# Performance work log

Measured on AMD Instinct MI355X. Metric: run time of the kernel, lower is better.

## Reference

```python
import jax, jax.numpy as jnp
import numpy as np

B, N, T, C, H, E = 4, 256, 36, 64, 4, 4096
D = C // H          # per-head dim
CH = 2 * C          # GAT hidden channels (embed_size * 2)


def _ln(x, g, b):
    mu = x.mean(-1, keepdims=True)
    v = ((x - mu) ** 2).mean(-1, keepdims=True)
    return (x - mu) / jnp.sqrt(v + 1e-5) * g + b


def _gat_conv(x, src, dst, W, a_s, a_d, b):
    # GATConv, heads=1, add_self_loops=False, negative_slope=0.2
    h = x @ W                                        # [N, F]
    e = jax.nn.leaky_relu((h * a_s).sum(-1)[src] + (h * a_d).sum(-1)[dst], 0.2)  # [E]
    m = jax.ops.segment_max(e, dst, num_segments=N)  # per-dst softmax (stable)
    w = jnp.exp(e - m[dst])
    s = jax.ops.segment_sum(w, dst, num_segments=N)
    alpha = w / (s[dst] + 1e-16)
    return jax.ops.segment_sum(h[src] * alpha[:, None], dst, num_segments=N) + b


def _forward(query, key, value, edge_attr, D_S, W_emb, b_emb, Wq, Wk, Wv, W_fc, b_fc,
             ln1_g, ln1_b, ln2_g, ln2_b, W_ff1, b_ff1, W_ff2, b_ff2,
             gat1_W, gat1_as, gat1_ad, gat1_b, gat2_W, gat2_as, gat2_ad, gat2_b,
             jk_W, jk_b, W_fs, b_fs, W_fg, b_fg, edge_index):
    src, dst = edge_index[0], edge_index[1]

    def gat(x):  # [N, C] -> [N, C]; 2-layer GAT with jk='max'
        h1 = jax.nn.relu(_gat_conv(x, src, dst, gat1_W, gat1_as, gat1_ad, gat1_b))
        h2 = jax.nn.relu(_gat_conv(h1, src, dst, gat2_W, gat2_as, gat2_ad, gat2_b))
        return jnp.maximum(h1, h2) @ jk_W + jk_b

    # GAT is applied to the ORIGINAL query (before D_S is added), once per timestep.
    xg = jax.vmap(jax.vmap(gat))(query.transpose(0, 2, 1, 3))  # [B, T, N, C]
    # source loop PREPENDS each timestep's output -> time axis is reversed
    X_G = xg[:, ::-1].transpose(0, 2, 1, 3)                    # [B, N, T, C]

    ds = (D_S @ W_emb + b_emb)[None, :, None, :]               # [1, N, 1, C]
    q = query + ds
    k = key + ds
    v = value + ds

    qh = q.reshape(B, N, T, H, D) @ Wq                         # per-head shared linear
    kh = k.reshape(B, N, T, H, D) @ Wk
    vh = v.reshape(B, N, T, H, D) @ Wv
    attn = jnp.einsum('bqthd,bkthd->bqkth', qh, kh)            # [B, N, N, T, H]
    # NOTE: source softmaxes over dim=1 (the QUERY axis), scaled by sqrt(embed_size)
    a = jax.nn.softmax(attn / jnp.sqrt(jnp.float32(C)), axis=1)
    o = jnp.einsum('bqkth,bkthd->bqthd', a, vh).reshape(B, N, T, C)
    o = o @ W_fc + b_fc

    M_s = _ln(o + q, ln1_g, ln1_b)                             # dropout p=0 (identity)
    ff = jax.nn.relu(M_s @ W_ff1 + b_ff1) @ W_ff2 + b_ff2
    U_s = _ln(ff + M_s, ln2_g, ln2_b)

    g = jax.nn.sigmoid(U_s @ W_fs + b_fs + X_G @ W_fg + b_fg)
    return g * U_s + (1.0 - g) * X_G


def setup_inputs():
    key = jax.random.key(0)
    ki = iter(jax.random.split(key, 64))

    def p(shape):
        fan = shape[0]
        return jax.random.normal(next(ki), shape, dtype=jnp.float32) / jnp.float32(float(np.sqrt(fan)))

    inp = {}
    inp['query'] = jax.random.normal(next(ki), (B, N, T, C), dtype=jnp.float32)
    inp['key'] = jax.random.normal(next(ki), (B, N, T, C), dtype=jnp.float32)
    inp['value'] = jax.random.normal(next(ki), (B, N, T, C), dtype=jnp.float32)
    inp['edge_attr'] = jax.random.normal(next(ki), (E,), dtype=jnp.float32)
    inp['D_S'] = jax.random.normal(next(ki), (N, N), dtype=jnp.float32)  # adj, learned param
    inp['W_emb'] = p((N, C)); inp['b_emb'] = jnp.zeros((C,), jnp.float32)
    inp['Wq'] = p((D, D)); inp['Wk'] = p((D, D)); inp['Wv'] = p((D, D))
    inp['W_fc'] = p((C, C)); inp['b_fc'] = jnp.zeros((C,), jnp.float32)
    inp['ln1_g'] = jnp.ones((C,), jnp.float32); inp['ln1_b'] = jnp.zeros((C,), jnp.float32)
    inp['ln2_g'] = jnp.ones((C,), jnp.float32); inp['ln2_b'] = jnp.zeros((C,), jnp.float32)
    inp['W_ff1'] = p((C, 4 * C)); inp['b_ff1'] = jnp.zeros((4 * C,), jnp.float32)
    inp['W_ff2'] = p((4 * C, C)); inp['b_ff2'] = jnp.zeros((C,), jnp.float32)
    inp['gat1_W'] = p((C, CH)); inp['gat1_as'] = p((CH,)); inp['gat1_ad'] = p((CH,)); inp['gat1_b'] = jnp.zeros((CH,), jnp.float32)
    inp['gat2_W'] = p((CH, CH)); inp['gat2_as'] = p((CH,)); inp['gat2_ad'] = p((CH,)); inp['gat2_b'] = jnp.zeros((CH,), jnp.float32)
    inp['jk_W'] = p((CH, C)); inp['jk_b'] = jnp.zeros((C,), jnp.float32)
    inp['W_fs'] = p((C, C)); inp['b_fs'] = jnp.zeros((C,), jnp.float32)
    inp['W_fg'] = p((C, C)); inp['b_fg'] = jnp.zeros((C,), jnp.float32)
    inp['edge_index'] = jax.random.randint(next(ki), (2, E), 0, N, dtype=jnp.int32)
    return inp


def reference(query, key, value, edge_attr, D_S, W_emb, b_emb, Wq, Wk, Wv, W_fc, b_fc,
              ln1_g, ln1_b, ln2_g, ln2_b, W_ff1, b_ff1, W_ff2, b_ff2,
              gat1_W, gat1_as, gat1_ad, gat1_b, gat2_W, gat2_as, gat2_ad, gat2_b,
              jk_W, jk_b, W_fs, b_fs, W_fg, b_fg, edge_index):
    return _forward(query, key, value, edge_attr, D_S, W_emb, b_emb, Wq, Wk, Wv, W_fc, b_fc,
                    ln1_g, ln1_b, ln2_g, ln2_b, W_ff1, b_ff1, W_ff2, b_ff2,
                    gat1_W, gat1_as, gat1_ad, gat1_b, gat2_W, gat2_as, gat2_ad, gat2_b,
                    jk_W, jk_b, W_fs, b_fs, W_fg, b_fg, edge_index)
```

## Files before the change

kernel.cpp:

```cpp
#include <hip/hip_runtime.h>

typedef unsigned short u16;
typedef unsigned int u32;

#define B_ 4
#define N_ 256
#define T_ 36
#define C_ 64
#define H_ 4
#define D_ 16
#define CH_ 128
#define E_ 4096
#define G_ (B_*T_)
#define TOK_ (B_*N_*T_)

#define DS_OFF  0
#define XG_OFF  (DS_OFF + N_*C_)
#define HA_OFF  (XG_OFF + TOK_*C_)
#define HB_OFF  (HA_OFF + G_*N_*CH_/2)
#define HS_OFF  (HB_OFF + G_*N_*CH_/2)
#define HD_OFF  (HS_OFF + G_*N_)
#define INT_OFF (HD_OFF + G_*N_)
#define MS_OFF  (INT_OFF + 4608)

__device__ __forceinline__ float bf2f(u16 u){
  u32 x = ((u32)u) << 16;
  return __builtin_bit_cast(float, x);
}
__device__ __forceinline__ u16 f2bf(float f){
  u32 x = __builtin_bit_cast(u32, f);
  x += 0x7fffu + ((x >> 16) & 1u);
  return (u16)(x >> 16);
}
__device__ __forceinline__ void unpack8(uint4 u, float* f){
  f[0]=bf2f((u16)(u.x & 0xffffu)); f[1]=bf2f((u16)(u.x >> 16));
  f[2]=bf2f((u16)(u.y & 0xffffu)); f[3]=bf2f((u16)(u.y >> 16));
  f[4]=bf2f((u16)(u.z & 0xffffu)); f[5]=bf2f((u16)(u.z >> 16));
  f[6]=bf2f((u16)(u.w & 0xffffu)); f[7]=bf2f((u16)(u.w >> 16));
}
__device__ __forceinline__ uint4 pack8f(const float* f){
  uint4 u;
  u.x = (u32)f2bf(f[0]) | ((u32)f2bf(f[1]) << 16);
  u.y = (u32)f2bf(f[2]) | ((u32)f2bf(f[3]) << 16);
  u.z = (u32)f2bf(f[4]) | ((u32)f2bf(f[5]) << 16);
  u.w = (u32)f2bf(f[6]) | ((u32)f2bf(f[7]) << 16);
  return u;
}
__device__ __forceinline__ int rfl(int v){ return __builtin_amdgcn_readfirstlane(v); }

__device__ __forceinline__ void gq_from_bid(int bid, int& g, int& q){
  int xc = bid & 7, slot = bid >> 3;
  q = slot & 3;
  g = xc + ((slot >> 2) << 3);
}

#define SP_ 20

__global__ __launch_bounds__(256)
void k_pre(const float* __restrict__ query, const float* __restrict__ W1,
           const float* __restrict__ as1, const float* __restrict__ ad1,
           u16* __restrict__ h, float* __restrict__ hs_ws, float* __restrict__ hd_ws,
           const float* __restrict__ DSm, const float* __restrict__ Wemb,
           const float* __restrict__ bemb, float* __restrict__ dsb,
           const int* __restrict__ ei, int* __restrict__ indptr, int* __restrict__ srcs)
{
  __shared__ union UP {
    struct { float xs[64][65]; float red[2][4][64]; } lin;
    struct { int srcL[E_]; int dstL[E_]; int tmp[E_]; int cnt[N_]; int base[N_+1]; } c;
  } S;
  const int bid = blockIdx.x;
  const int tid = threadIdx.x;

  if (bid < 576){
    int g, q; gq_from_bid(bid, g, q);
    const int n0 = q * 64;
    const int b = g / T_, t = g % T_;
    {
      const size_t gb = (((size_t)b*N_ + n0)*T_ + t)*C_;
      #pragma unroll
      for (int it = 0; it < 4; it++){
        int idx = tid + 256*it;
        int row = idx >> 4, c4 = (idx & 15) * 4;
        float4 v = *(const float4*)(query + gb + (size_t)row*(T_*C_) + c4);
        S.lin.xs[row][c4+0] = v.x; S.lin.xs[row][c4+1] = v.y;
        S.lin.xs[row][c4+2] = v.z; S.lin.xs[row][c4+3] = v.w;
      }
    }
    __syncthreads();

    const int r = tid & 63;
    const int cb = rfl(tid >> 6);
    const int ch0 = cb * 32;

    float acc[32];
    #pragma unroll
    for (int j = 0; j < 32; j++) acc[j] = 0.f;
    for (int k = 0; k < 64; k++){
      float xv = S.lin.xs[r][k];
      const float* wrow = W1 + k*CH_ + ch0;
      #pragma unroll
      for (int j = 0; j < 32; j++) acc[j] += xv * wrow[j];
    }
    float hs = 0.f, hd = 0.f;
    #pragma unroll
    for (int j = 0; j < 32; j++){ hs += acc[j]*as1[ch0+j]; hd += acc[j]*ad1[ch0+j]; }
    S.lin.red[0][cb][r] = hs; S.lin.red[1][cb][r] = hd;

    u16* hp = h + ((size_t)(g*N_ + n0 + r))*CH_ + ch0;
    #pragma unroll
    for (int j8 = 0; j8 < 32; j8 += 8)
      *(uint4*)(hp + j8) = pack8f(&acc[j8]);

    __syncthreads();
    if (tid < 64){
      float a = S.lin.red[0][0][tid]+S.lin.red[0][1][tid]+S.lin.red[0][2][tid]+S.lin.red[0][3][tid];
      float d = S.lin.red[1][0][tid]+S.lin.red[1][1][tid]+S.lin.red[1][2][tid]+S.lin.red[1][3][tid];
      hs_ws[g*N_ + n0 + tid] = a;
      hd_ws[g*N_ + n0 + tid] = d;
    }
  } else if (bid < 640){
    const int n = (bid - 576) * 4 + (tid >> 6);
    const int c = tid & 63;
    float acc = bemb[c];
    for (int m = 0; m < N_; m++) acc += DSm[n*N_ + m] * Wemb[m*C_ + c];
    dsb[n*C_ + c] = acc;
  } else {
    for (int e = tid; e < E_; e += 256){ S.c.srcL[e] = ei[e]; S.c.dstL[e] = ei[E_ + e]; }
    S.c.cnt[tid] = 0;
    __syncthreads();
    for (int e = tid; e < E_; e += 256) atomicAdd(&S.c.cnt[S.c.dstL[e]], 1);
    __syncthreads();
    if (tid == 0){
      int run = 0;
      for (int i = 0; i < N_; i++){ S.c.base[i] = run; run += S.c.cnt[i]; }
      S.c.base[N_] = run;
    }
    __syncthreads();
    S.c.cnt[tid] = 0;
    __syncthreads();
    for (int e = tid; e < E_; e += 256){
      int d = S.c.dstL[e];
      int p = atomicAdd(&S.c.cnt[d], 1);
      S.c.tmp[S.c.base[d] + p] = e;
    }
    __syncthreads();
    {
      const int p0 = S.c.base[tid], p1 = S.c.base[tid] + S.c.cnt[tid];
      for (int i = p0 + 1; i < p1; i++){
        int v = S.c.tmp[i]; int j = i - 1;
        while (j >= p0 && S.c.tmp[j] > v){ S.c.tmp[j+1] = S.c.tmp[j]; j--; }
        S.c.tmp[j+1] = v;
      }
      for (int j = p0; j < p1; j++) srcs[j] = S.c.srcL[S.c.tmp[j]];
    }
    indptr[tid] = S.c.base[tid];
    if (tid == 0) indptr[N_] = S.c.base[N_];
  }
}

__global__ __launch_bounds__(256)
void k_agg1(const u16* __restrict__ hin, const float* __restrict__ hs_ws, const float* __restrict__ hd_ws,
            const int* __restrict__ indptr, const int* __restrict__ srcs,
            const float* __restrict__ bias, u16* __restrict__ hout)
{
  __shared__ int   srcs_l[E_];
  __shared__ float alpha_l[E_];
  __shared__ float hs_l[N_];
  const int bid = blockIdx.x;
  int g, q; gq_from_bid(bid, g, q);
  const int n0 = q * 64;
  const int tid = threadIdx.x;

  const int p00 = indptr[n0];
  const int pend = indptr[n0 + 64];
  const int cntE = pend - p00;
  for (int i = tid; i < cntE; i += 256) srcs_l[i] = srcs[p00 + i];
  hs_l[tid] = hs_ws[g*N_ + tid];
  __syncthreads();

  if (tid < 64){
    const int dst = n0 + tid;
    const int p0 = indptr[dst] - p00, p1 = indptr[dst+1] - p00;
    const float hdn = hd_ws[g*N_ + dst];
    for (int j = p0; j < p1; j++){
      float e = hs_l[srcs_l[j]] + hdn;
      alpha_l[j] = e > 0.f ? e : 0.2f * e;
    }
    float m = -1e30f;
    for (int j = p0; j < p1; j++) m = fmaxf(m, alpha_l[j]);
    float s = 0.f;
    for (int j = p0; j < p1; j++){
      float w = __expf(alpha_l[j] - m);
      alpha_l[j] = w; s += w;
    }
    float inv = 1.f / (s + 1e-16f);
    for (int j = p0; j < p1; j++) alpha_l[j] *= inv;
  }
  __syncthreads();

  const int r = tid & 63;
  const int cb = rfl(tid >> 6);
  const int ch0 = cb * 32;
  const int dst = n0 + r;
  const int p0 = indptr[dst] - p00, p1 = indptr[dst+1] - p00;

  float acc[32];
  #pragma unroll
  for (int j = 0; j < 32; j++) acc[j] = 0.f;
  for (int j = p0; j < p1; j++){
    float a = alpha_l[j];
    int s = srcs_l[j];
    const uint4* hp = (const uint4*)(hin + ((size_t)(g*N_ + s))*CH_ + ch0);
    #pragma unroll
    for (int qq = 0; qq < 4; qq++){
      float hv[8]; unpack8(hp[qq], hv);
      #pragma unroll
      for (int i = 0; i < 8; i++) acc[qq*8+i] += a * hv[i];
    }
  }
  float o[32];
  #pragma unroll
  for (int j = 0; j < 32; j++){
    float v = acc[j] + bias[ch0+j];
    o[j] = v > 0.f ? v : 0.f;
  }
  u16* op = hout + ((size_t)(g*N_ + dst))*CH_ + ch0;
  #pragma unroll
  for (int j8 = 0; j8 < 32; j8 += 8)
    *(uint4*)(op + j8) = pack8f(&o[j8]);
}

__global__ __launch_bounds__(256)
void k_lin2(const u16* __restrict__ h1, const float* __restrict__ W2,
            const float* __restrict__ as2, const float* __restrict__ ad2,
            u16* __restrict__ h2, float* __restrict__ hs_ws, float* __restrict__ hd_ws)
{
  __shared__ float xs[64][129];
  __shared__ float red[2][4][64];
  const int bid = blockIdx.x;
  int g, q; gq_from_bid(bid, g, q);
  const int n0 = q * 64;
  const int tid = threadIdx.x;

  {
    #pragma unroll
    for (int it = 0; it < 4; it++){
      int idx = tid + 256*it;
      int row = idx >> 4, c8 = (idx & 15) * 8;
      uint4 u = *(const uint4*)(h1 + ((size_t)(g*N_ + n0 + row))*CH_ + c8);
      float v[8]; unpack8(u, v);
      #pragma unroll
      for (int i = 0; i < 8; i++) xs[row][c8+i] = v[i];
    }
  }
  __syncthreads();

  const int r = tid & 63;
  const int cb = rfl(tid >> 6);
  const int ch0 = cb * 32;

  float acc[32];
  #pragma unroll
  for (int j = 0; j < 32; j++) acc[j] = 0.f;
  for (int k = 0; k < 128; k++){
    float xv = xs[r][k];
    const float* wrow = W2 + k*CH_ + ch0;
    #pragma unroll
    for (int j = 0; j < 32; j++) acc[j] += xv * wrow[j];
  }
  float hs = 0.f, hd = 0.f;
  #pragma unroll
  for (int j = 0; j < 32; j++){ hs += acc[j]*as2[ch0+j]; hd += acc[j]*ad2[ch0+j]; }
  red[0][cb][r] = hs; red[1][cb][r] = hd;

  u16* hp = h2 + ((size_t)(g*N_ + n0 + r))*CH_ + ch0;
  #pragma unroll
  for (int j8 = 0; j8 < 32; j8 += 8)
    *(uint4*)(hp + j8) = pack8f(&acc[j8]);

  __syncthreads();
  if (tid < 64){
    float a = red[0][0][tid]+red[0][1][tid]+red[0][2][tid]+red[0][3][tid];
    float d = red[1][0][tid]+red[1][1][tid]+red[1][2][tid]+red[1][3][tid];
    hs_ws[g*N_ + n0 + tid] = a;
    hd_ws[g*N_ + n0 + tid] = d;
  }
}

__global__ __launch_bounds__(256)
void k_aggjk(const u16* __restrict__ h2, const float* __restrict__ hs_ws, const float* __restrict__ hd_ws,
             const int* __restrict__ indptr, const int* __restrict__ srcs,
             const float* __restrict__ b2, const u16* __restrict__ h1,
             const float* __restrict__ jkW, const float* __restrict__ jkb, float* __restrict__ xg,
             const float* __restrict__ query, const float* __restrict__ key,
             const float* __restrict__ Wq, const float* __restrict__ Wk,
             const float* __restrict__ dsb, float* __restrict__ mS)
{
  __shared__ union UJ {
    struct { int srcs_l[E_]; float alpha_l[E_]; float hs_l[N_]; } a;
    struct { float xs[64][129]; } l;
    struct { float qs[N_][SP_]; float wq[16][16]; float wk[16][16]; } s;
  } U;
  const int bid = blockIdx.x;
  const int tid = threadIdx.x;

  if (bid < 576){
    int g, q; gq_from_bid(bid, g, q);
    const int n0 = q * 64;
    const int b = g / T_, t = g % T_;

    const int p00 = indptr[n0];
    const int pend = indptr[n0 + 64];
    const int cntE = pend - p00;
    for (int i = tid; i < cntE; i += 256) U.a.srcs_l[i] = srcs[p00 + i];
    U.a.hs_l[tid] = hs_ws[g*N_ + tid];
    __syncthreads();

    if (tid < 64){
      const int dst = n0 + tid;
      const int p0 = indptr[dst] - p00, p1 = indptr[dst+1] - p00;
      const float hdn = hd_ws[g*N_ + dst];
      for (int j = p0; j < p1; j++){
        float e = U.a.hs_l[U.a.srcs_l[j]] + hdn;
        U.a.alpha_l[j] = e > 0.f ? e : 0.2f * e;
      }
      float m = -1e30f;
      for (int j = p0; j < p1; j++) m = fmaxf(m, U.a.alpha_l[j]);
      float s = 0.f;
      for (int j = p0; j < p1; j++){
        float w = __expf(U.a.alpha_l[j] - m);
        U.a.alpha_l[j] = w; s += w;
      }
      float inv = 1.f / (s + 1e-16f);
      for (int j = p0; j < p1; j++) U.a.alpha_l[j] *= inv;
    }
    __syncthreads();

    const int r = tid & 63;
    const int cb = rfl(tid >> 6);
    const int ch0 = cb * 32;
    const int dst = n0 + r;
    const int p0 = indptr[dst] - p00, p1 = indptr[dst+1] - p00;

    float acc[32];
    #pragma unroll
    for (int j = 0; j < 32; j++) acc[j] = 0.f;
    for (int j = p0; j < p1; j++){
      float a = U.a.alpha_l[j];
      int s = U.a.srcs_l[j];
      const uint4* hp = (const uint4*)(h2 + ((size_t)(g*N_ + s))*CH_ + ch0);
      #pragma unroll
      for (int qq = 0; qq < 4; qq++){
        float hv[8]; unpack8(hp[qq], hv);
        #pragma unroll
        for (int i = 0; i < 8; i++) acc[qq*8+i] += a * hv[i];
      }
    }
    float o[32];
    {
      const uint4* h1p = (const uint4*)(h1 + ((size_t)(g*N_ + dst))*CH_ + ch0);
      #pragma unroll
      for (int j8 = 0; j8 < 32; j8 += 8){
        float h1v[8]; unpack8(h1p[j8>>3], h1v);
        #pragma unroll
        for (int i = 0; i < 8; i++){
          float v = acc[j8+i] + b2[ch0+j8+i];
          v = v > 0.f ? v : 0.f;
          o[j8+i] = fmaxf(h1v[i], v);
        }
      }
    }
    __syncthreads();

    #pragma unroll
    for (int j = 0; j < 32; j++) U.l.xs[r][ch0+j] = o[j];
    __syncthreads();

    const int o0 = cb * 16;
    float acc2[16];
    #pragma unroll
    for (int j = 0; j < 16; j++) acc2[j] = 0.f;
    for (int k = 0; k < 128; k++){
      float xv = U.l.xs[r][k];
      const float* wrow = jkW + k*C_ + o0;
      #pragma unroll
      for (int j = 0; j < 16; j++) acc2[j] += xv * wrow[j];
    }
    float* op = xg + ((((size_t)b*N_ + n0 + r)*T_) + (T_-1-t))*C_ + o0;
    #pragma unroll
    for (int j4 = 0; j4 < 16; j4 += 4){
      float4 v = make_float4(acc2[j4]+jkb[o0+j4], acc2[j4+1]+jkb[o0+j4+1],
                             acc2[j4+2]+jkb[o0+j4+2], acc2[j4+3]+jkb[o0+j4+3]);
      *(float4*)(op + j4) = v;
    }
  } else {
    const int sb = bid - 576;
    const int b = sb / (T_*H_);
    const int rem = sb % (T_*H_);
    const int t = rem / H_;
    const int h = rem % H_;
    const int n = tid;

    U.s.wq[n>>4][n&15] = Wq[n];
    U.s.wk[n>>4][n&15] = Wk[n];

    const size_t base = ((((size_t)b*N_ + n)*T_) + t)*C_ + h*D_;
    const float* dsp = dsb + n*C_ + h*D_;

    float x[16];
    #pragma unroll
    for (int j4 = 0; j4 < 16; j4 += 4){
      float4 a = *(const float4*)(query + base + j4);
      float4 d = *(const float4*)(dsp + j4);
      x[j4]=a.x+d.x; x[j4+1]=a.y+d.y; x[j4+2]=a.z+d.z; x[j4+3]=a.w+d.w;
    }
    __syncthreads();
    #pragma unroll
    for (int j = 0; j < 16; j++){
      float a = 0.f;
      #pragma unroll
      for (int i = 0; i < 16; i++) a += x[i]*U.s.wq[i][j];
      U.s.qs[n][j] = a;
    }
    float khr[16];
    #pragma unroll
    for (int j4 = 0; j4 < 16; j4 += 4){
      float4 a = *(const float4*)(key + base + j4);
      float4 d = *(const float4*)(dsp + j4);
      x[j4]=a.x+d.x; x[j4+1]=a.y+d.y; x[j4+2]=a.z+d.z; x[j4+3]=a.w+d.w;
    }
    #pragma unroll
    for (int j = 0; j < 16; j++){
      float a = 0.f;
      #pragma unroll
      for (int i = 0; i < 16; i++) a += x[i]*U.s.wk[i][j];
      khr[j] = a;
    }
    __syncthreads();

    float m[4], s[4];
    #pragma unroll
    for (int c = 0; c < 4; c++){ m[c] = -1e30f; s[c] = 0.f; }
    for (int qq = 0; qq < 64; qq++){
      #pragma unroll
      for (int c = 0; c < 4; c++){
        const float* qrow = &U.s.qs[qq + 64*c][0];
        float4 a0 = *(const float4*)(qrow);
        float4 a1 = *(const float4*)(qrow+4);
        float4 a2 = *(const float4*)(qrow+8);
        float4 a3 = *(const float4*)(qrow+12);
        float d = a0.x*khr[0]+a0.y*khr[1]+a0.z*khr[2]+a0.w*khr[3]
                + a1.x*khr[4]+a1.y*khr[5]+a1.z*khr[6]+a1.w*khr[7]
                + a2.x*khr[8]+a2.y*khr[9]+a2.z*khr[10]+a2.w*khr[11]
                + a3.x*khr[12]+a3.y*khr[13]+a3.z*khr[14]+a3.w*khr[15];
        d *= 0.125f;
        float mn = fmaxf(m[c], d);
        s[c] = s[c]*__expf(m[c]-mn) + __expf(d-mn);
        m[c] = mn;
      }
    }
    float M = fmaxf(fmaxf(m[0],m[1]), fmaxf(m[2],m[3]));
    float S = s[0]*__expf(m[0]-M) + s[1]*__expf(m[1]-M)
            + s[2]*__expf(m[2]-M) + s[3]*__expf(m[3]-M);
    mS[(size_t)sb*512 + n*2]     = M;
    mS[(size_t)sb*512 + n*2 + 1] = 1.f / S;
  }
}

__global__ __launch_bounds__(256)
void k_av(const float* __restrict__ query, const float* __restrict__ key, const float* __restrict__ value,
          const float* __restrict__ Wq, const float* __restrict__ Wk, const float* __restrict__ Wv,
          const float* __restrict__ dsb, const float* __restrict__ mS, float* __restrict__ o_ws)
{
  __shared__ float ks[N_][SP_];
  __shared__ float vs[N_][SP_];
  __shared__ float2 msl[N_];
  __shared__ float wq[16][16], wk[16][16], wv[16][16];

  const int bx = blockIdx.x;
  const int b = bx / (T_*H_);
  const int rem = bx % (T_*H_);
  const int t = rem / H_;
  const int h = rem % H_;
  const int n = threadIdx.x;

  wq[n>>4][n&15] = Wq[n];
  wk[n>>4][n&15] = Wk[n];
  wv[n>>4][n&15] = Wv[n];
  msl[n] = *(const float2*)(mS + (size_t)bx*512 + n*2);

  const size_t base = ((((size_t)b*N_ + n)*T_) + t)*C_ + h*D_;
  const float* dsp = dsb + n*C_ + h*D_;

  float ds16[16];
  #pragma unroll
  for (int j4 = 0; j4 < 16; j4 += 4){
    float4 d = *(const float4*)(dsp + j4);
    ds16[j4]=d.x; ds16[j4+1]=d.y; ds16[j4+2]=d.z; ds16[j4+3]=d.w;
  }
  __syncthreads();

  float x[16];
  #pragma unroll
  for (int j4 = 0; j4 < 16; j4 += 4){
    float4 a = *(const float4*)(key + base + j4);
    x[j4]=a.x+ds16[j4]; x[j4+1]=a.y+ds16[j4+1]; x[j4+2]=a.z+ds16[j4+2]; x[j4+3]=a.w+ds16[j4+3];
  }
  #pragma unroll
  for (int j = 0; j < 16; j++){
    float a = 0.f;
    #pragma unroll
    for (int i = 0; i < 16; i++) a += x[i]*wk[i][j];
    ks[n][j] = a;
  }
  #pragma unroll
  for (int j4 = 0; j4 < 16; j4 += 4){
    float4 a = *(const float4*)(value + base + j4);
    x[j4]=a.x+ds16[j4]; x[j4+1]=a.y+ds16[j4+1]; x[j4+2]=a.z+ds16[j4+2]; x[j4+3]=a.w+ds16[j4+3];
  }
  #pragma unroll
  for (int j = 0; j < 16; j++){
    float a = 0.f;
    #pragma unroll
    for (int i = 0; i < 16; i++) a += x[i]*wv[i][j];
    vs[n][j] = a;
  }
  float qhr[16];
  #pragma unroll
  for (int j4 = 0; j4 < 16; j4 += 4){
    float4 a = *(const float4*)(query + base + j4);
    x[j4]=a.x+ds16[j4]; x[j4+1]=a.y+ds16[j4+1]; x[j4+2]=a.z+ds16[j4+2]; x[j4+3]=a.w+ds16[j4+3];
  }
  #pragma unroll
  for (int j = 0; j < 16; j++){
    float a = 0.f;
    #pragma unroll
    for (int i = 0; i < 16; i++) a += x[i]*wq[i][j];
    qhr[j] = a;
  }
  __syncthreads();

  float o0[16], o1[16];
  #pragma unroll
  for (int j = 0; j < 16; j++){ o0[j] = 0.f; o1[j] = 0.f; }
  for (int k = 0; k < N_; k += 2){
    {
      const float* krow = &ks[k][0];
      float4 a0 = *(const float4*)(krow);
      float4 a1 = *(const float4*)(krow+4);
      float4 a2 = *(const float4*)(krow+8);
      float4 a3 = *(const float4*)(krow+12);
      float d = a0.x*qhr[0]+a0.y*qhr[1]+a0.z*qhr[2]+a0.w*qhr[3]
              + a1.x*qhr[4]+a1.y*qhr[5]+a1.z*qhr[6]+a1.w*qhr[7]
              + a2.x*qhr[8]+a2.y*qhr[9]+a2.z*qhr[10]+a2.w*qhr[11]
              + a3.x*qhr[12]+a3.y*qhr[13]+a3.z*qhr[14]+a3.w*qhr[15];
      float2 ms0 = msl[k];
      float p = __expf(d*0.125f - ms0.x) * ms0.y;
      const float* vrow = &vs[k][0];
      float4 v0 = *(const float4*)(vrow);
      float4 v1 = *(const float4*)(vrow+4);
      float4 v2 = *(const float4*)(vrow+8);
      float4 v3 = *(const float4*)(vrow+12);
      o0[0]+=p*v0.x; o0[1]+=p*v0.y; o0[2]+=p*v0.z; o0[3]+=p*v0.w;
      o0[4]+=p*v1.x; o0[5]+=p*v1.y; o0[6]+=p*v1.z; o0[7]+=p*v1.w;
      o0[8]+=p*v2.x; o0[9]+=p*v2.y; o0[10]+=p*v2.z; o0[11]+=p*v2.w;
      o0[12]+=p*v3.x; o0[13]+=p*v3.y; o0[14]+=p*v3.z; o0[15]+=p*v3.w;
    }
    {
      const float* krow = &ks[k+1][0];
      float4 a0 = *(const float4*)(krow);
      float4 a1 = *(const float4*)(krow+4);
      float4 a2 = *(const float4*)(krow+8);
      float4 a3 = *(const float4*)(krow+12);
      float d = a0.x*qhr[0]+a0.y*qhr[1]+a0.z*qhr[2]+a0.w*qhr[3]
              + a1.x*qhr[4]+a1.y*qhr[5]+a1.z*qhr[6]+a1.w*qhr[7]
              + a2.x*qhr[8]+a2.y*qhr[9]+a2.z*qhr[10]+a2.w*qhr[11]
              + a3.x*qhr[12]+a3.y*qhr[13]+a3.z*qhr[14]+a3.w*qhr[15];
      float2 ms1 = msl[k+1];
      float p = __expf(d*0.125f - ms1.x) * ms1.y;
      const float* vrow = &vs[k+1][0];
      float4 v0 = *(const float4*)(vrow);
      float4 v1 = *(const float4*)(vrow+4);
      float4 v2 = *(const float4*)(vrow+8);
      float4 v3 = *(const float4*)(vrow+12);
      o1[0]+=p*v0.x; o1[1]+=p*v0.y; o1[2]+=p*v0.z; o1[3]+=p*v0.w;
      o1[4]+=p*v1.x; o1[5]+=p*v1.y; o1[6]+=p*v1.z; o1[7]+=p*v1.w;
      o1[8]+=p*v2.x; o1[9]+=p*v2.y; o1[10]+=p*v2.z; o1[11]+=p*v2.w;
      o1[12]+=p*v3.x; o1[13]+=p*v3.y; o1[14]+=p*v3.z; o1[15]+=p*v3.w;
    }
  }
  float* op = o_ws + base;
  #pragma unroll
  for (int j4 = 0; j4 < 16; j4 += 4)
    *(float4*)(op + j4) = make_float4(o0[j4]+o1[j4], o0[j4+1]+o1[j4+1],
                                      o0[j4+2]+o1[j4+2], o0[j4+3]+o1[j4+3]);
}

__global__ __launch_bounds__(256)
void k_final(const float* __restrict__ query, const float* __restrict__ dsb,
             const float* __restrict__ o_ws, const float* __restrict__ xg_ws,
             const float* __restrict__ Wfc, const float* __restrict__ bfc,
             const float* __restrict__ ln1g, const float* __restrict__ ln1b,
             const float* __restrict__ ln2g, const float* __restrict__ ln2b,
             const float* __restrict__ Wff1, const float* __restrict__ bff1,
             const float* __restrict__ Wff2, const float* __restrict__ bff2,
             const float* __restrict__ Wfs, const float* __restrict__ bfs,
             const float* __restrict__ Wfg, const float* __restrict__ bfg,
             float* __restrict__ out)
{
  __shared__ u16 smA[64*66];
  __shared__ u16 smB[64*66];
  __shared__ union UH { u16 h[128*66]; float o[64*66]; } HH;
  __shared__ float lnxA[4][64];
  __shared__ float lnxB[4][64];

  const int tid = threadIdx.x;
  const int token0 = blockIdx.x * 64;
  const int w = rfl(tid >> 6);
  const int tok = tid & 63;
  const int c0 = w * 16;

  #pragma unroll
  for (int it = 0; it < 4; it++){
    int idx = tid + 256*it;
    int tk = idx >> 4, c4 = (idx & 15) * 4;
    int gtok = token0 + tk;
    int n = (gtok / T_) & (N_-1);
    float4 ov = *(const float4*)(o_ws + (size_t)gtok*C_ + c4);
    float4 qv = *(const float4*)(query + (size_t)gtok*C_ + c4);
    float4 dv = *(const float4*)(dsb + n*C_ + c4);
    smA[(c4+0)*66+tk] = f2bf(ov.x); smA[(c4+1)*66+tk] = f2bf(ov.y);
    smA[(c4+2)*66+tk] = f2bf(ov.z); smA[(c4+3)*66+tk] = f2bf(ov.w);
    smB[(c4+0)*66+tk] = f2bf(qv.x+dv.x); smB[(c4+1)*66+tk] = f2bf(qv.y+dv.y);
    smB[(c4+2)*66+tk] = f2bf(qv.z+dv.z); smB[(c4+3)*66+tk] = f2bf(qv.w+dv.w);
  }
  __syncthreads();

  float x1[16];
  #pragma unroll
  for (int j = 0; j < 16; j++) x1[j] = 0.f;
  for (int i = 0; i < C_; i++){
    float ov = bf2f(smA[i*66 + tok]);
    const float* wrow = Wfc + i*C_ + c0;
    #pragma unroll
    for (int j = 0; j < 16; j++) x1[j] += ov * wrow[j];
  }
  #pragma unroll
  for (int j = 0; j < 16; j++) x1[j] += bfc[c0+j] + bf2f(smB[(c0+j)*66 + tok]);

  float s1 = 0.f;
  #pragma unroll
  for (int j = 0; j < 16; j++) s1 += x1[j];
  lnxA[w][tok] = s1;
  __syncthreads();
  float mu = (lnxA[0][tok]+lnxA[1][tok]+lnxA[2][tok]+lnxA[3][tok]) * (1.f/64.f);
  float v1 = 0.f;
  #pragma unroll
  for (int j = 0; j < 16; j++){ float d = x1[j]-mu; v1 += d*d; }
  lnxB[w][tok] = v1;
  __syncthreads();
  float var = (lnxB[0][tok]+lnxB[1][tok]+lnxB[2][tok]+lnxB[3][tok]) * (1.f/64.f);
  float rstd = rsqrtf(var + 1e-5f);
  float ms[16];
  #pragma unroll
  for (int j = 0; j < 16; j++) ms[j] = (x1[j]-mu)*rstd*ln1g[c0+j] + ln1b[c0+j];
  __syncthreads();
  #pragma unroll
  for (int j = 0; j < 16; j++) smB[(c0+j)*66 + tok] = f2bf(ms[j]);
  __syncthreads();

  float part[16];
  #pragma unroll
  for (int j = 0; j < 16; j++) part[j] = 0.f;
  #pragma unroll
  for (int ch = 0; ch < 2; ch++){
    float fch[32];
    #pragma unroll
    for (int kk = 0; kk < 32; kk++) fch[kk] = 0.f;
    const int kbase = w*64 + ch*32;
    for (int i = 0; i < C_; i++){
      float msv = bf2f(smB[i*66 + tok]);
      const float* wrow = Wff1 + i*(4*C_) + kbase;
      #pragma unroll
      for (int kk = 0; kk < 32; kk++) fch[kk] += msv * wrow[kk];
    }
    #pragma unroll
    for (int kk = 0; kk < 32; kk++){
      float v = fch[kk] + bff1[kbase+kk];
      fch[kk] = v > 0.f ? v : 0.f;
    }
    if (ch) __syncthreads();
    #pragma unroll
    for (int kk = 0; kk < 32; kk++) HH.h[(w*32+kk)*66 + tok] = f2bf(fch[kk]);
    __syncthreads();
    #pragma unroll
    for (int wq = 0; wq < 4; wq++){
      #pragma unroll 8
      for (int kk = 0; kk < 32; kk++){
        int k = wq*64 + ch*32 + kk;
        float hv = bf2f(HH.h[(wq*32+kk)*66 + tok]);
        const float* wrow = Wff2 + k*C_ + c0;
        #pragma unroll
        for (int j = 0; j < 16; j++) part[j] += hv * wrow[j];
      }
    }
  }
  float x2[16];
  #pragma unroll
  for (int j = 0; j < 16; j++) x2[j] = part[j] + bff2[c0+j] + ms[j];

  float s2 = 0.f;
  #pragma unroll
  for (int j = 0; j < 16; j++) s2 += x2[j];
  __syncthreads();
  lnxA[w][tok] = s2;
  __syncthreads();
  float mu2 = (lnxA[0][tok]+lnxA[1][tok]+lnxA[2][tok]+lnxA[3][tok]) * (1.f/64.f);
  float v2 = 0.f;
  #pragma unroll
  for (int j = 0; j < 16; j++){ float d = x2[j]-mu2; v2 += d*d; }
  lnxB[w][tok] = v2;
  __syncthreads();
  float var2 = (lnxB[0][tok]+lnxB[1][tok]+lnxB[2][tok]+lnxB[3][tok]) * (1.f/64.f);
  float rstd2 = rsqrtf(var2 + 1e-5f);
  float us[16];
  #pragma unroll
  for (int j = 0; j < 16; j++) us[j] = (x2[j]-mu2)*rstd2*ln2g[c0+j] + ln2b[c0+j];

  #pragma unroll
  for (int j = 0; j < 16; j++) smA[(c0+j)*66 + tok] = f2bf(us[j]);
  #pragma unroll
  for (int it = 0; it < 4; it++){
    int idx = tid + 256*it;
    int tk = idx >> 4, c4 = (idx & 15) * 4;
    int gtok = token0 + tk;
    float4 xv = *(const float4*)(xg_ws + (size_t)gtok*C_ + c4);
    HH.h[(c4+0)*66+tk] = f2bf(xv.x); HH.h[(c4+1)*66+tk] = f2bf(xv.y);
    HH.h[(c4+2)*66+tk] = f2bf(xv.z); HH.h[(c4+3)*66+tk] = f2bf(xv.w);
  }
  __syncthreads();

  float ga[16];
  #pragma unroll
  for (int j = 0; j < 16; j++) ga[j] = 0.f;
  for (int i = 0; i < C_; i++){
    float uv = bf2f(smA[i*66 + tok]);
    float xv = bf2f(HH.h[i*66 + tok]);
    const float* wsr = Wfs + i*C_ + c0;
    const float* wgr = Wfg + i*C_ + c0;
    #pragma unroll
    for (int j = 0; j < 16; j++) ga[j] += uv*wsr[j] + xv*wgr[j];
  }
  float res[16];
  #pragma unroll
  for (int j = 0; j < 16; j++){
    float a = ga[j] + bfs[c0+j] + bfg[c0+j];
    float gg = 1.f / (1.f + __expf(-a));
    float xgv = bf2f(HH.h[(c0+j)*66 + tok]);
    res[j] = gg*us[j] + (1.f-gg)*xgv;
  }
  __syncthreads();
  #pragma unroll
  for (int j = 0; j < 16; j++) HH.o[(c0+j)*66 + tok] = res[j];
  __syncthreads();
  #pragma unroll
  for (int it = 0; it < 4; it++){
    int idx = tid + 256*it;
    int tk = idx >> 4, c4 = (idx & 15) * 4;
    int gtok = token0 + tk;
    float4 v = make_float4(HH.o[(c4+0)*66+tk], HH.o[(c4+1)*66+tk],
                           HH.o[(c4+2)*66+tk], HH.o[(c4+3)*66+tk]);
    *(float4*)(out + (size_t)gtok*C_ + c4) = v;
  }
}

extern "C" void kernel_launch(void* const* d_in, const int* in_sizes, int n_in,
                              void* d_out, int out_size, void* d_ws, size_t ws_size,
                              hipStream_t stream)
{
  (void)in_sizes; (void)n_in; (void)out_size; (void)ws_size;
  const float* query = (const float*)d_in[0];
  const float* key   = (const float*)d_in[1];
  const float* value = (const float*)d_in[2];
  const float* DSm   = (const float*)d_in[4];
  const float* Wemb  = (const float*)d_in[5];
  const float* bemb  = (const float*)d_in[6];
  const float* Wq    = (const float*)d_in[7];
  const float* Wk    = (const float*)d_in[8];
  const float* Wv    = (const float*)d_in[9];
  const float* Wfc   = (const float*)d_in[10];
  const float* bfc   = (const float*)d_in[11];
  const float* ln1g  = (const float*)d_in[12];
  const float* ln1b  = (const float*)d_in[13];
  const float* ln2g  = (const float*)d_in[14];
  const float* ln2b  = (const float*)d_in[15];
  const float* Wff1  = (const float*)d_in[16];
  const float* bff1  = (const float*)d_in[17];
  const float* Wff2  = (const float*)d_in[18];
  const float* bff2  = (const float*)d_in[19];
  const float* g1W   = (const float*)d_in[20];
  const float* g1as  = (const float*)d_in[21];
  const float* g1ad  = (const float*)d_in[22];
  const float* g1b   = (const float*)d_in[23];
  const float* g2W   = (const float*)d_in[24];
  const float* g2as  = (const float*)d_in[25];
  const float* g2ad  = (const float*)d_in[26];
  const float* g2b   = (const float*)d_in[27];
  const float* jkW   = (const float*)d_in[28];
  const float* jkb   = (const float*)d_in[29];
  const float* Wfs   = (const float*)d_in[30];
  const float* bfs   = (const float*)d_in[31];
  const float* Wfg   = (const float*)d_in[32];
  const float* bfg   = (const float*)d_in[33];
  const int* ei      = (const int*)d_in[34];
  float* out = (float*)d_out;

  float* wf     = (float*)d_ws;
  float* dsb    = wf + DS_OFF;
  float* xg_ws  = wf + XG_OFF;
  u16*   hA     = (u16*)(wf + HA_OFF);
  u16*   hB     = (u16*)(wf + HB_OFF);
  float* o_ws   = wf + HA_OFF;
  float* hs_ws  = wf + HS_OFF;
  float* hd_ws  = wf + HD_OFF;
  int*   indptr = (int*)(wf + INT_OFF);
  int*   srcs   = indptr + 260;
  float* mS     = wf + MS_OFF;

  k_pre  <<<dim3(641),  dim3(256), 0, stream>>>(query, g1W, g1as, g1ad, hA, hs_ws, hd_ws,
                                                DSm, Wemb, bemb, dsb, ei, indptr, srcs);
  k_agg1 <<<dim3(576),  dim3(256), 0, stream>>>(hA, hs_ws, hd_ws, indptr, srcs, g1b, hB);
  k_lin2 <<<dim3(576),  dim3(256), 0, stream>>>(hB, g2W, g2as, g2ad, hA, hs_ws, hd_ws);
  k_aggjk<<<dim3(1152), dim3(256), 0, stream>>>(hA, hs_ws, hd_ws, indptr, srcs, g2b, hB,
                                                jkW, jkb, xg_ws,
                                                query, key, Wq, Wk, dsb, mS);
  k_av   <<<dim3(576),  dim3(256), 0, stream>>>(query, key, value, Wq, Wk, Wv, dsb, mS, o_ws);
  k_final<<<dim3(576),  dim3(256), 0, stream>>>(query, dsb, o_ws, xg_ws,
      Wfc, bfc, ln1g, ln1b, ln2g, ln2b,
      Wff1, bff1, Wff2, bff2,
      Wfs, bfs, Wfg, bfg, out);
}
```

Measured before the change: 322.6 us.

## Parallelize GAT edge softmax across four lanes per node and shrink LDS

Replaces the single-thread-per-destination edge softmax (only 64 of 256 threads active) with four lanes per destination that reduce max and sum through wave shuffles. Shrinks the per-block shared edge buffers from E to a fixed quarter-range cap (1408), and stores the JK input tile in LDS as bf16 with vector loads instead of fp32 scalars. Together these aim to raise utilization and occupancy in the aggregation kernels. The fixed edge cap will overflow if a 64-node quarter ever receives more edges than the cap, and the bf16 staging adds rounding to the JK linear layer.

```diff
diff --git a/kernel.cpp b/kernel.cpp
--- a/kernel.cpp
+++ b/kernel.cpp
@@ -11,6 +11,7 @@
 #define D_ 16
 #define CH_ 128
 #define E_ 4096
+#define EQ_ 1408
 #define G_ (B_*T_)
 #define TOK_ (B_*N_*T_)
 
@@ -55,6 +56,36 @@
 }
 
 #define SP_ 20
+
+__device__ __forceinline__ void edge_softmax_par(int tid, int n0,
+    const int* __restrict__ indptr, int p00,
+    const int* srcs_l, const float* hs_l, const float* __restrict__ hd_ws,
+    int g, float* alpha_l)
+{
+  const int ld = tid >> 2;
+  const int sl = tid & 3;
+  const int dst = n0 + ld;
+  const int p0 = indptr[dst] - p00, p1 = indptr[dst+1] - p00;
+  const float hdn = hd_ws[g*N_ + dst];
+  float m = -1e30f;
+  for (int j = p0 + sl; j < p1; j += 4){
+    float e = hs_l[srcs_l[j]] + hdn;
+    e = e > 0.f ? e : 0.2f * e;
+    alpha_l[j] = e;
+    m = fmaxf(m, e);
+  }
+  m = fmaxf(m, __shfl_xor(m, 1, 64));
+  m = fmaxf(m, __shfl_xor(m, 2, 64));
+  float s = 0.f;
+  for (int j = p0 + sl; j < p1; j += 4){
+    float w = __expf(alpha_l[j] - m);
+    alpha_l[j] = w; s += w;
+  }
+  s += __shfl_xor(s, 1, 64);
+  s += __shfl_xor(s, 2, 64);
+  float inv = 1.f / (s + 1e-16f);
+  for (int j = p0 + sl; j < p1; j += 4) alpha_l[j] *= inv;
+}
 
 __global__ __launch_bounds__(256)
 void k_pre(const float* __restrict__ query, const float* __restrict__ W1,
@@ -163,8 +194,8 @@
             const int* __restrict__ indptr, const int* __restrict__ srcs,
             const float* __restrict__ bias, u16* __restrict__ hout)
 {
-  __shared__ int   srcs_l[E_];
-  __shared__ float alpha_l[E_];
+  __shared__ int   srcs_l[EQ_];
+  __shared__ float alpha_l[EQ_];
   __shared__ float hs_l[N_];
   const int bid = blockIdx.x;
   int g, q; gq_from_bid(bid, g, q);
@@ -178,24 +209,7 @@
   hs_l[tid] = hs_ws[g*N_ + tid];
   __syncthreads();
 
-  if (tid < 64){
-    const int dst = n0 + tid;
-    const int p0 = indptr[dst] - p00, p1 = indptr[dst+1] - p00;
-    const float hdn = hd_ws[g*N_ + dst];
-    for (int j = p0; j < p1; j++){
-      float e = hs_l[srcs_l[j]] + hdn;
-      alpha_l[j] = e > 0.f ? e : 0.2f * e;
-    }
-    float m = -1e30f;
-    for (int j = p0; j < p1; j++) m = fmaxf(m, alpha_l[j]);
-    float s = 0.f;
-    for (int j = p0; j < p1; j++){
-      float w = __expf(alpha_l[j] - m);
-      alpha_l[j] = w; s += w;
-    }
-    float inv = 1.f / (s + 1e-16f);
-    for (int j = p0; j < p1; j++) alpha_l[j] *= inv;
-  }
+  edge_softmax_par(tid, n0, indptr, p00, srcs_l, hs_l, hd_ws, g, alpha_l);
   __syncthreads();
 
   const int r = tid & 63;
@@ -297,8 +311,8 @@
              const float* __restrict__ dsb, float* __restrict__ mS)
 {
   __shared__ union UJ {
-    struct { int srcs_l[E_]; float alpha_l[E_]; float hs_l[N_]; } a;
-    struct { float xs[64][129]; } l;
+    struct { int srcs_l[EQ_]; float alpha_l[EQ_]; float hs_l[N_]; } a;
+    struct { u16 xs[64][136]; } l;
     struct { float qs[N_][SP_]; float wq[16][16]; float wk[16][16]; } s;
   } U;
   const int bid = blockIdx.x;
@@ -316,24 +330,7 @@
     U.a.hs_l[tid] = hs_ws[g*N_ + tid];
     __syncthreads();
 
-    if (tid < 64){
-      const int dst = n0 + tid;
-      const int p0 = indptr[dst] - p00, p1 = indptr[dst+1] - p00;
-      const float hdn = hd_ws[g*N_ + dst];
-      for (int j = p0; j < p1; j++){
-        float e = U.a.hs_l[U.a.srcs_l[j]] + hdn;
-        U.a.alpha_l[j] = e > 0.f ? e : 0.2f * e;
-      }
-      float m = -1e30f;
-      for (int j = p0; j < p1; j++) m = fmaxf(m, U.a.alpha_l[j]);
-      float s = 0.f;
-      for (int j = p0; j < p1; j++){
-        float w = __expf(U.a.alpha_l[j] - m);
-        U.a.alpha_l[j] = w; s += w;
-      }
-      float inv = 1.f / (s + 1e-16f);
-      for (int j = p0; j < p1; j++) U.a.alpha_l[j] *= inv;
-    }
+    edge_softmax_par(tid, n0, indptr, p00, U.a.srcs_l, U.a.hs_l, hd_ws, g, U.a.alpha_l);
     __syncthreads();
 
     const int r = tid & 63;
@@ -373,18 +370,23 @@
     __syncthreads();
 
     #pragma unroll
-    for (int j = 0; j < 32; j++) U.l.xs[r][ch0+j] = o[j];
+    for (int j8 = 0; j8 < 32; j8 += 8)
+      *(uint4*)&U.l.xs[r][ch0 + j8] = pack8f(&o[j8]);
     __syncthreads();
 
     const int o0 = cb * 16;
     float acc2[16];
     #pragma unroll
     for (int j = 0; j < 16; j++) acc2[j] = 0.f;
-    for (int k = 0; k < 128; k++){
-      float xv = U.l.xs[r][k];
-      const float* wrow = jkW + k*C_ + o0;
-      #pragma unroll
-      for (int j = 0; j < 16; j++) acc2[j] += xv * wrow[j];
+    for (int k8 = 0; k8 < 16; k8++){
+      uint4 u = *(const uint4*)&U.l.xs[r][k8*8];
+      float hv[8]; unpack8(u, hv);
+      #pragma unroll
+      for (int kk = 0; kk < 8; kk++){
+        const float* wrow = jkW + (k8*8+kk)*C_ + o0;
+        #pragma unroll
+        for (int j = 0; j < 16; j++) acc2[j] += hv[kk] * wrow[j];
+      }
     }
     float* op = xg + ((((size_t)b*N_ + n0 + r)*T_) + (T_-1-t))*C_ + o0;
     #pragma unroll
```

Result: faster. 304.6 us (-5.6%).
